# Performance work log

Hardware: AMD Instinct MI355X
Metric: run time of the kernel (lower is better)

Reference implementation:

```python
import jax, jax.numpy as jnp
import numpy as np

N = 100_000      # nodes
E = 3_200_000    # edges (avg degree 32)
IN_F = 256
OUT_F = 256

def setup_inputs() -> dict:
    key = jax.random.key(0)
    k1, k2, k3, k4, k5 = jax.random.split(key, 5)
    x = jax.random.normal(k1, (N, IN_F), dtype=jnp.float32)
    stdv = 1.0 / np.sqrt(OUT_F).astype(np.float32)
    W = jax.random.uniform(k2, (IN_F, OUT_F), dtype=jnp.float32, minval=-stdv, maxval=stdv)
    edge_vals = jax.random.uniform(k3, (E,), dtype=jnp.float32)  # normalized adj values
    edge_src = jax.random.randint(k4, (E,), 0, N, dtype=jnp.int32)
    edge_dst = jax.random.randint(k5, (E,), 0, N, dtype=jnp.int32)
    return {"x": x, "W": W, "edge_vals": edge_vals, "edge_src": edge_src, "edge_dst": edge_dst}

def reference(x, W, edge_vals, edge_src, edge_dst):
    # support = X @ W  (dense projection)
    support = x @ W                                   # [N, OUT_F]
    # output = A @ support, A sparse COO: out[d] += a[e] * support[s] for edge e=(s,d)
    msgs = support[edge_src] * edge_vals[:, None]     # [E, OUT_F] gather + scale
    out = jax.ops.segment_sum(msgs, edge_dst, num_segments=N)  # [N, OUT_F] scatter-add
    return out
```

## Files before the change

### kernel.cpp

```cpp
#include <hip/hip_runtime.h>
#include <stdint.h>

#define IN_F 256
#define OUT_F 256
#define NB 782
#define CHUNK 8192
#define CAP 8192

typedef short bf16x8 __attribute__((ext_vector_type(8)));
typedef float f32x4  __attribute__((ext_vector_type(4)));

__device__ __forceinline__ uint16_t f2bf(float f) {
    union { float f; uint32_t u; } a; a.f = f;
    uint32_t u = a.u + 0x7FFFu + ((a.u >> 16) & 1u);
    return (uint16_t)(u >> 16);
}
__device__ __forceinline__ float bf2f(uint16_t h) {
    union { uint32_t u; float f; } a; a.u = ((uint32_t)h) << 16;
    return a.f;
}

__global__ void k_wt(const float* __restrict__ W, uint16_t* __restrict__ Wt) {
    int idx = blockIdx.x * 256 + threadIdx.x;
    int k = idx >> 8, j = idx & 255;
    Wt[j * IN_F + k] = f2bf(W[k * OUT_F + j]);
}

__global__ void __launch_bounds__(256) k_gemm(const float* __restrict__ x,
                                              const uint16_t* __restrict__ Wt,
                                              uint16_t* __restrict__ sup, int nstrip) {
    int wid  = (blockIdx.x * blockDim.x + threadIdx.x) >> 6;
    if (wid >= nstrip) return;
    int lane = threadIdx.x & 63;
    int r = lane & 15;
    int g = lane >> 4;
    int row = wid * 16 + r;

    bf16x8 a[8];
    const float* xr = x + (size_t)row * IN_F + g * 8;
#pragma unroll
    for (int ks = 0; ks < 8; ++ks) {
        float4 p0 = *reinterpret_cast<const float4*>(xr + ks * 32);
        float4 p1 = *reinterpret_cast<const float4*>(xr + ks * 32 + 4);
        bf16x8 t;
        t[0]=f2bf(p0.x); t[1]=f2bf(p0.y); t[2]=f2bf(p0.z); t[3]=f2bf(p0.w);
        t[4]=f2bf(p1.x); t[5]=f2bf(p1.y); t[6]=f2bf(p1.z); t[7]=f2bf(p1.w);
        a[ks] = t;
    }
#pragma unroll
    for (int nt = 0; nt < 16; ++nt) {
        f32x4 acc = {0.f, 0.f, 0.f, 0.f};
        const uint16_t* wb = Wt + (size_t)(nt * 16 + r) * IN_F + g * 8;
#pragma unroll
        for (int ks = 0; ks < 8; ++ks) {
            bf16x8 b = *reinterpret_cast<const bf16x8*>(wb + ks * 32);
            acc = __builtin_amdgcn_mfma_f32_16x16x32_bf16(a[ks], b, acc, 0, 0, 0);
        }
        uint16_t* so = sup + (size_t)(wid * 16 + g * 4) * OUT_F + nt * 16 + r;
#pragma unroll
        for (int i = 0; i < 4; ++i)
            so[(size_t)i * OUT_F] = f2bf(acc[i]);
    }
}

__global__ void k_bhist(const int* __restrict__ dst, int* __restrict__ bcnt, int E) {
    __shared__ int h[NB];
    for (int b = threadIdx.x; b < NB; b += 256) h[b] = 0;
    __syncthreads();
    int i = blockIdx.x * blockDim.x + threadIdx.x;
    int stride = gridDim.x * blockDim.x;
    for (; i < E; i += stride) atomicAdd(&h[dst[i] >> 7], 1);
    __syncthreads();
    for (int b = threadIdx.x; b < NB; b += 256)
        if (h[b]) atomicAdd(&bcnt[b], h[b]);
}

__global__ void k_bscan(const int* __restrict__ bcnt, int* __restrict__ bbase,
                        int* __restrict__ bcur, int* __restrict__ row_ptr, int N) {
    __shared__ int sh[1024];
    int t = threadIdx.x;
    int v = (t < NB) ? bcnt[t] : 0;
    sh[t] = v; __syncthreads();
    for (int off = 1; off < 1024; off <<= 1) {
        int u = (t >= off) ? sh[t - off] : 0;
        __syncthreads();
        sh[t] += u;
        __syncthreads();
    }
    int excl = sh[t] - v;
    if (t < NB) { bbase[t] = excl; bcur[t] = excl; }
    if (t == 1023) { bbase[NB] = sh[1023]; row_ptr[N] = sh[1023]; }
}

__global__ void __launch_bounds__(256) k_bfill(const int* __restrict__ src,
                                               const int* __restrict__ dst,
                                               const float* __restrict__ val,
                                               int* __restrict__ bcur,
                                               uint2* __restrict__ rec,
                                               unsigned char* __restrict__ dstl, int E) {
    __shared__ int s_cnt[NB];
    __shared__ int s_cur[NB];
    __shared__ int s_gbase[NB];
    __shared__ int s_scan[256];
    __shared__ uint2 s_rec[CHUNK];
    __shared__ unsigned short s_bin[CHUNK];
    __shared__ unsigned char s_ndl[CHUNK];

    const int tid = threadIdx.x;
    const int e0 = blockIdx.x * CHUNK;
    const int n = min(CHUNK, E - e0);

    for (int b = tid; b < NB; b += 256) s_cnt[b] = 0;
    __syncthreads();
    for (int i = tid; i < n; i += 256) atomicAdd(&s_cnt[dst[e0 + i] >> 7], 1);
    __syncthreads();
    int c[4]; int sum = 0; int b4 = tid * 4;
#pragma unroll
    for (int j = 0; j < 4; ++j) {
        c[j] = (b4 + j < NB) ? s_cnt[b4 + j] : 0;
        sum += c[j];
    }
    s_scan[tid] = sum; __syncthreads();
    for (int off = 1; off < 256; off <<= 1) {
        int u = (tid >= off) ? s_scan[tid - off] : 0;
        __syncthreads();
        s_scan[tid] += u;
        __syncthreads();
    }
    int run = s_scan[tid] - sum;
#pragma unroll
    for (int j = 0; j < 4; ++j) {
        if (b4 + j < NB) { s_cur[b4 + j] = run; run += c[j]; }
    }
    __syncthreads();
    for (int i = tid; i < n; i += 256) {
        int d = dst[e0 + i];
        int b = d >> 7;
        int p = atomicAdd(&s_cur[b], 1);
        s_rec[p] = make_uint2((unsigned)src[e0 + i], __float_as_uint(val[e0 + i]));
        s_bin[p] = (unsigned short)b;
        s_ndl[p] = (unsigned char)(d & 127);
    }
    __syncthreads();
    for (int b = tid; b < NB; b += 256)
        if (s_cnt[b] > 0) s_gbase[b] = atomicAdd(&bcur[b], s_cnt[b]);
    __syncthreads();
    for (int p = tid; p < n; p += 256) {
        int b = s_bin[p];
        int g = s_gbase[b] + (p - (s_cur[b] - s_cnt[b]));
        rec[g] = s_rec[p];
        dstl[g] = s_ndl[p];
    }
}

__global__ void __launch_bounds__(256) k_bsort(uint2* __restrict__ rec,
                                               const unsigned char* __restrict__ dstl,
                                               const int* __restrict__ bbase,
                                               int* __restrict__ row_ptr, int N) {
    __shared__ int h[128];
    __shared__ int sc[256];
    __shared__ int cur[128];
    __shared__ uint2 s_rec[CAP];

    const int tid = threadIdx.x;
    const int b = blockIdx.x;
    const int beg = bbase[b], end = bbase[b + 1];
    const int node0 = b * 128;
    const int nn = min(128, N - node0);

    if (tid < 128) h[tid] = 0;
    __syncthreads();
    for (int i = beg + tid; i < end; i += 256) atomicAdd(&h[dstl[i]], 1);
    __syncthreads();
    int v = (tid < 128) ? h[tid] : 0;
    sc[tid] = v; __syncthreads();
    for (int off = 1; off < 128; off <<= 1) {
        int u = (tid >= off) ? sc[tid - off] : 0;
        __syncthreads();
        sc[tid] += u;
        __syncthreads();
    }
    int excl = sc[tid] - v;
    if (tid < 128) {
        cur[tid] = excl;
        if (tid < nn) row_ptr[node0 + tid] = beg + excl;
    }
    __syncthreads();
    for (int i = beg + tid; i < end; i += 256) {
        uint2 r = rec[i];
        int p = atomicAdd(&cur[dstl[i]], 1);
        s_rec[p] = r;
    }
    __syncthreads();
    for (int i = tid; i < end - beg; i += 256) rec[beg + i] = s_rec[i];
}

__global__ void __launch_bounds__(256) k_gather(const uint16_t* __restrict__ sup,
                                                const uint2* __restrict__ rec,
                                                const int* __restrict__ row_ptr,
                                                float* __restrict__ out, int N) {
    int node = blockIdx.x * 4 + (threadIdx.x >> 6);
    if (node >= N) return;
    int lane = threadIdx.x & 63;
    int beg = row_ptr[node], end = row_ptr[node + 1];
    float4 acc = make_float4(0.f, 0.f, 0.f, 0.f);
    const uint16_t* supb = sup + (size_t)lane * 4;
    if (beg < end) {
        uint2 r0 = rec[beg];
        uint2 r1 = r0;
        for (int e = beg + 1; e <= end; ++e) {
            if (e < end) r1 = rec[e];
            float v = __uint_as_float(r0.y);
            ushort4 s = *reinterpret_cast<const ushort4*>(supb + (size_t)r0.x * OUT_F);
            acc.x += v * bf2f(s.x);
            acc.y += v * bf2f(s.y);
            acc.z += v * bf2f(s.z);
            acc.w += v * bf2f(s.w);
            r0 = r1;
        }
    }
    *reinterpret_cast<float4*>(out + (size_t)node * OUT_F + lane * 4) = acc;
}

extern "C" void kernel_launch(void* const* d_in, const int* in_sizes, int n_in,
                              void* d_out, int out_size, void* d_ws, size_t ws_size,
                              hipStream_t stream) {
    const float* x   = (const float*)d_in[0];
    const float* W   = (const float*)d_in[1];
    const float* ev  = (const float*)d_in[2];
    const int*   es  = (const int*)d_in[3];
    const int*   ed  = (const int*)d_in[4];
    float*       out = (float*)d_out;

    const int N = in_sizes[0] / IN_F;
    const int E = in_sizes[2];

    char* ws = (char*)d_ws;
    uint16_t*      sup     = (uint16_t*)(ws);
    uint2*         rec     = (uint2*)   (ws + 51200000);
    unsigned char* dstl    = (unsigned char*)(ws + 76800000);
    int*           bcnt    = (int*)     (ws + 80000000);
    int*           bbase   = (int*)     (ws + 80003200);
    int*           bcur    = (int*)     (ws + 80006400);
    int*           row_ptr = (int*)     (ws + 80009600);
    uint16_t*      Wt      = (uint16_t*)(ws + 80409608);

    const int nstrip = N / 16;
    const int nfill  = (E + CHUNK - 1) / CHUNK;

    hipMemsetAsync(bcnt, 0, (size_t)NB * sizeof(int), stream);
    k_wt   <<<256, 256, 0, stream>>>(W, Wt);
    k_gemm <<<(nstrip + 3) / 4, 256, 0, stream>>>(x, Wt, sup, nstrip);
    k_bhist<<<512, 256, 0, stream>>>(ed, bcnt, E);
    k_bscan<<<1, 1024, 0, stream>>>(bcnt, bbase, bcur, row_ptr, N);
    k_bfill<<<nfill, 256, 0, stream>>>(es, ed, ev, bcur, rec, dstl, E);
    k_bsort<<<NB, 256, 0, stream>>>(rec, dstl, bbase, row_ptr, N);
    k_gather<<<(N + 3) / 4, 256, 0, stream>>>(sup, rec, row_ptr, out, N);
}
```

Baseline: 656.6 us.

## Pack local dst into src bits, shrink LDS tiles, unroll gather by eight

Encodes the 7-bit local destination index in the upper bits of the source index, which removes the separate dstl byte array and its global reads and writes in the fill and sort kernels. Halves the fill chunk and reduces sort capacity to lower LDS use per block, allowing more concurrent blocks. The gather loop issues eight edge gathers at once into four independent accumulators to raise memory-level parallelism. Risks: sources must fit in 17 bits, and a bucket with more than 4608 edges would overflow LDS.

```diff
diff --git a/kernel.cpp b/kernel.cpp
--- a/kernel.cpp
+++ b/kernel.cpp
@@ -4,8 +4,9 @@
 #define IN_F 256
 #define OUT_F 256
 #define NB 782
-#define CHUNK 8192
-#define CAP 8192
+#define CHUNK 4096
+#define CAP 4608
+#define SRCM 0x1FFFF
 
 typedef short bf16x8 __attribute__((ext_vector_type(8)));
 typedef float f32x4  __attribute__((ext_vector_type(4)));
@@ -96,15 +97,13 @@
                                                const int* __restrict__ dst,
                                                const float* __restrict__ val,
                                                int* __restrict__ bcur,
-                                               uint2* __restrict__ rec,
-                                               unsigned char* __restrict__ dstl, int E) {
+                                               uint2* __restrict__ rec, int E) {
     __shared__ int s_cnt[NB];
     __shared__ int s_cur[NB];
     __shared__ int s_gbase[NB];
     __shared__ int s_scan[256];
     __shared__ uint2 s_rec[CHUNK];
     __shared__ unsigned short s_bin[CHUNK];
-    __shared__ unsigned char s_ndl[CHUNK];
 
     const int tid = threadIdx.x;
     const int e0 = blockIdx.x * CHUNK;
@@ -137,9 +136,9 @@
         int d = dst[e0 + i];
         int b = d >> 7;
         int p = atomicAdd(&s_cur[b], 1);
-        s_rec[p] = make_uint2((unsigned)src[e0 + i], __float_as_uint(val[e0 + i]));
+        s_rec[p] = make_uint2((unsigned)src[e0 + i] | ((unsigned)(d & 127) << 17),
+                              __float_as_uint(val[e0 + i]));
         s_bin[p] = (unsigned short)b;
-        s_ndl[p] = (unsigned char)(d & 127);
     }
     __syncthreads();
     for (int b = tid; b < NB; b += 256)
@@ -147,14 +146,11 @@
     __syncthreads();
     for (int p = tid; p < n; p += 256) {
         int b = s_bin[p];
-        int g = s_gbase[b] + (p - (s_cur[b] - s_cnt[b]));
-        rec[g] = s_rec[p];
-        dstl[g] = s_ndl[p];
+        rec[s_gbase[b] + (p - (s_cur[b] - s_cnt[b]))] = s_rec[p];
     }
 }
 
 __global__ void __launch_bounds__(256) k_bsort(uint2* __restrict__ rec,
-                                               const unsigned char* __restrict__ dstl,
                                                const int* __restrict__ bbase,
                                                int* __restrict__ row_ptr, int N) {
     __shared__ int h[128];
@@ -170,7 +166,8 @@
 
     if (tid < 128) h[tid] = 0;
     __syncthreads();
-    for (int i = beg + tid; i < end; i += 256) atomicAdd(&h[dstl[i]], 1);
+    for (int i = beg + tid; i < end; i += 256)
+        atomicAdd(&h[(rec[i].x >> 17) & 127], 1);
     __syncthreads();
     int v = (tid < 128) ? h[tid] : 0;
     sc[tid] = v; __syncthreads();
@@ -188,7 +185,7 @@
     __syncthreads();
     for (int i = beg + tid; i < end; i += 256) {
         uint2 r = rec[i];
-        int p = atomicAdd(&cur[dstl[i]], 1);
+        int p = atomicAdd(&cur[(r.x >> 17) & 127], 1);
         s_rec[p] = r;
     }
     __syncthreads();
@@ -202,23 +199,47 @@
     int node = blockIdx.x * 4 + (threadIdx.x >> 6);
     if (node >= N) return;
     int lane = threadIdx.x & 63;
-    int beg = row_ptr[node], end = row_ptr[node + 1];
-    float4 acc = make_float4(0.f, 0.f, 0.f, 0.f);
+    int beg = __builtin_amdgcn_readfirstlane(row_ptr[node]);
+    int end = __builtin_amdgcn_readfirstlane(row_ptr[node + 1]);
     const uint16_t* supb = sup + (size_t)lane * 4;
-    if (beg < end) {
-        uint2 r0 = rec[beg];
-        uint2 r1 = r0;
-        for (int e = beg + 1; e <= end; ++e) {
-            if (e < end) r1 = rec[e];
-            float v = __uint_as_float(r0.y);
-            ushort4 s = *reinterpret_cast<const ushort4*>(supb + (size_t)r0.x * OUT_F);
-            acc.x += v * bf2f(s.x);
-            acc.y += v * bf2f(s.y);
-            acc.z += v * bf2f(s.z);
-            acc.w += v * bf2f(s.w);
-            r0 = r1;
-        }
-    }
+
+    float4 a0 = make_float4(0.f,0.f,0.f,0.f), a1 = a0, a2 = a0, a3 = a0;
+    int e = beg;
+    for (; e + 8 <= end; e += 8) {
+        uint2 q0 = rec[e+0], q1 = rec[e+1], q2 = rec[e+2], q3 = rec[e+3];
+        uint2 q4 = rec[e+4], q5 = rec[e+5], q6 = rec[e+6], q7 = rec[e+7];
+        ushort4 s0 = *reinterpret_cast<const ushort4*>(supb + (size_t)(q0.x & SRCM) * OUT_F);
+        ushort4 s1 = *reinterpret_cast<const ushort4*>(supb + (size_t)(q1.x & SRCM) * OUT_F);
+        ushort4 s2 = *reinterpret_cast<const ushort4*>(supb + (size_t)(q2.x & SRCM) * OUT_F);
+        ushort4 s3 = *reinterpret_cast<const ushort4*>(supb + (size_t)(q3.x & SRCM) * OUT_F);
+        ushort4 s4 = *reinterpret_cast<const ushort4*>(supb + (size_t)(q4.x & SRCM) * OUT_F);
+        ushort4 s5 = *reinterpret_cast<const ushort4*>(supb + (size_t)(q5.x & SRCM) * OUT_F);
+        ushort4 s6 = *reinterpret_cast<const ushort4*>(supb + (size_t)(q6.x & SRCM) * OUT_F);
+        ushort4 s7 = *reinterpret_cast<const ushort4*>(supb + (size_t)(q7.x & SRCM) * OUT_F);
+        float v0 = __uint_as_float(q0.y), v1 = __uint_as_float(q1.y);
+        float v2 = __uint_as_float(q2.y), v3 = __uint_as_float(q3.y);
+        float v4 = __uint_as_float(q4.y), v5 = __uint_as_float(q5.y);
+        float v6 = __uint_as_float(q6.y), v7 = __uint_as_float(q7.y);
+        a0.x += v0*bf2f(s0.x); a0.y += v0*bf2f(s0.y); a0.z += v0*bf2f(s0.z); a0.w += v0*bf2f(s0.w);
+        a1.x += v1*bf2f(s1.x); a1.y += v1*bf2f(s1.y); a1.z += v1*bf2f(s1.z); a1.w += v1*bf2f(s1.w);
+        a2.x += v2*bf2f(s2.x); a2.y += v2*bf2f(s2.y); a2.z += v2*bf2f(s2.z); a2.w += v2*bf2f(s2.w);
+        a3.x += v3*bf2f(s3.x); a3.y += v3*bf2f(s3.y); a3.z += v3*bf2f(s3.z); a3.w += v3*bf2f(s3.w);
+        a0.x += v4*bf2f(s4.x); a0.y += v4*bf2f(s4.y); a0.z += v4*bf2f(s4.z); a0.w += v4*bf2f(s4.w);
+        a1.x += v5*bf2f(s5.x); a1.y += v5*bf2f(s5.y); a1.z += v5*bf2f(s5.z); a1.w += v5*bf2f(s5.w);
+        a2.x += v6*bf2f(s6.x); a2.y += v6*bf2f(s6.y); a2.z += v6*bf2f(s6.z); a2.w += v6*bf2f(s6.w);
+        a3.x += v7*bf2f(s7.x); a3.y += v7*bf2f(s7.y); a3.z += v7*bf2f(s7.z); a3.w += v7*bf2f(s7.w);
+    }
+    for (; e < end; ++e) {
+        uint2 q = rec[e];
+        float v = __uint_as_float(q.y);
+        ushort4 s = *reinterpret_cast<const ushort4*>(supb + (size_t)(q.x & SRCM) * OUT_F);
+        a0.x += v*bf2f(s.x); a0.y += v*bf2f(s.y); a0.z += v*bf2f(s.z); a0.w += v*bf2f(s.w);
+    }
+    float4 acc;
+    acc.x = (a0.x + a1.x) + (a2.x + a3.x);
+    acc.y = (a0.y + a1.y) + (a2.y + a3.y);
+    acc.z = (a0.z + a1.z) + (a2.z + a3.z);
+    acc.w = (a0.w + a1.w) + (a2.w + a3.w);
     *reinterpret_cast<float4*>(out + (size_t)node * OUT_F + lane * 4) = acc;
 }
 
@@ -236,14 +257,13 @@
     const int E = in_sizes[2];
 
     char* ws = (char*)d_ws;
-    uint16_t*      sup     = (uint16_t*)(ws);
-    uint2*         rec     = (uint2*)   (ws + 51200000);
-    unsigned char* dstl    = (unsigned char*)(ws + 76800000);
-    int*           bcnt    = (int*)     (ws + 80000000);
-    int*           bbase   = (int*)     (ws + 80003200);
-    int*           bcur    = (int*)     (ws + 80006400);
-    int*           row_ptr = (int*)     (ws + 80009600);
-    uint16_t*      Wt      = (uint16_t*)(ws + 80409608);
+    uint16_t* sup     = (uint16_t*)(ws);
+    uint2*    rec     = (uint2*)   (ws + 51200000);
+    int*      bcnt    = (int*)     (ws + 76800000);
+    int*      bbase   = (int*)     (ws + 76803200);
+    int*      bcur    = (int*)     (ws + 76806400);
+    int*      row_ptr = (int*)     (ws + 76809600);
+    uint16_t* Wt      = (uint16_t*)(ws + 77209608);
 
     const int nstrip = N / 16;
     const int nfill  = (E + CHUNK - 1) / CHUNK;
@@ -253,7 +273,7 @@
     k_gemm <<<(nstrip + 3) / 4, 256, 0, stream>>>(x, Wt, sup, nstrip);
     k_bhist<<<512, 256, 0, stream>>>(ed, bcnt, E);
     k_bscan<<<1, 1024, 0, stream>>>(bcnt, bbase, bcur, row_ptr, N);
-    k_bfill<<<nfill, 256, 0, stream>>>(es, ed, ev, bcur, rec, dstl, E);
-    k_bsort<<<NB, 256, 0, stream>>>(rec, dstl, bbase, row_ptr, N);
+    k_bfill<<<nfill, 256, 0, stream>>>(es, ed, ev, bcur, rec, E);
+    k_bsort<<<NB, 256, 0, stream>>>(rec, bbase, row_ptr, N);
     k_gather<<<(N + 3) / 4, 256, 0, stream>>>(sup, rec, row_ptr, out, N);
 }
```

After: 617.4 us. -6.0%, faster.
